# Kernel tuning notes

Hardware: AMD Instinct MI355X
Metric: run time of the kernel (lower is better)

The kernel has to match this reference:

```python
import jax, jax.numpy as jnp
import numpy as np

B, TGT, SRC, SRC_DIM, TGT_DIM = 4, 4096, 4096, 256, 256
NEG_BIG = 1.0e11   # additive mask constant from the torch code
CLAMP_MIN = -1.0e10


def setup_inputs() -> dict:
    key = jax.random.key(0)
    k1, k2, k3, k4 = jax.random.split(key, 4)
    h_t = jax.random.normal(k1, (B, TGT, TGT_DIM), dtype=jnp.float32)
    h_s = jax.random.normal(k2, (B, SRC, SRC_DIM), dtype=jnp.float32)
    m_s = jax.random.randint(k3, (B, SRC), 0, 2, dtype=jnp.int32)
    # linear_in: nn.Linear(src_dim, tgt_dim, bias=False) -> weight [tgt_dim, src_dim]
    lim = float(np.sqrt(1.0 / SRC_DIM))
    W_in = jax.random.uniform(k4, (TGT_DIM, SRC_DIM), dtype=jnp.float32, minval=-lim, maxval=lim)
    return {"h_t": h_t, "h_s": h_s, "m_s": m_s, "W_in": W_in}


def reference(h_t, h_s, m_s, W_in):
    # 'general' score: h_t @ (linear_in(h_s))^T
    energy = jnp.einsum("bsd,td->bst", h_s, W_in)          # (B, S, tgt_dim)
    scores = jnp.einsum("btd,bsd->bts", h_t, energy)        # (B, T, S)
    m = m_s.astype(scores.dtype)[:, None, :]                 # (B, 1, S)
    scores = scores * m - NEG_BIG * (1.0 - m)
    scores = jax.nn.softmax(jnp.maximum(scores, CLAMP_MIN), axis=-1)
    context = jnp.einsum("bts,bsd->btd", scores, h_s)        # (B, T, src_dim)
    return context, scores
```

## Files before the change

kernel.cpp:

```cpp
#include <hip/hip_runtime.h>
#include <cstdint>
#include <cstddef>

typedef _Float16 f16;
typedef _Float16 half8 __attribute__((ext_vector_type(8)));
typedef float floatx4 __attribute__((ext_vector_type(4)));

__device__ __forceinline__ void gload_lds16(const void* g, void* l) {
    __builtin_amdgcn_global_load_lds(
        (const __attribute__((address_space(1))) void*)g,
        (__attribute__((address_space(3))) void*)l,
        16, 0, 0);
}

__global__ void k_cvt(const float* __restrict__ src, f16* __restrict__ dst, int n8) {
    int i = blockIdx.x * blockDim.x + threadIdx.x;
    if (i >= n8) return;
    const float4* s = (const float4*)src + 2 * (size_t)i;
    float4 a = s[0], b = s[1];
    half8 h;
    h[0] = (f16)a.x; h[1] = (f16)a.y; h[2] = (f16)a.z; h[3] = (f16)a.w;
    h[4] = (f16)b.x; h[5] = (f16)b.y; h[6] = (f16)b.z; h[7] = (f16)b.w;
    ((half8*)dst)[i] = h;
}

__global__ void k_hs(const float* __restrict__ hs, f16* __restrict__ hs16, f16* __restrict__ hsT) {
    int id = blockIdx.x;
    int dt = id & 3;
    int st = (id >> 2) & 63;
    int b  = id >> 8;
    __shared__ f16 tile[64][65];
    int t = threadIdx.x;
    int s0 = st * 64, d0 = dt * 64;
#pragma unroll
    for (int i = 0; i < 16; i++) {
        int e = t + i * 256;
        int r = e >> 6, c = e & 63;
        float v = hs[((size_t)(b * 4096 + s0 + r)) * 256 + d0 + c];
        f16 hv = (f16)v;
        hs16[((size_t)(b * 4096 + s0 + r)) * 256 + d0 + c] = hv;
        tile[r][c] = hv;
    }
    __syncthreads();
#pragma unroll
    for (int i = 0; i < 16; i++) {
        int e = t + i * 256;
        int r = e >> 6, c = e & 63;
        hsT[((size_t)(b * 256 + d0 + r)) * 4096 + s0 + c] = tile[c][r];
    }
}

__global__ __launch_bounds__(256, 2) void k_energy(
    const f16* __restrict__ A,
    const f16* __restrict__ Bt,
    f16* __restrict__ C)
{
    int id = blockIdx.x;
    int tn = id & 1, tm = (id >> 1) & 31, b = id >> 6;
    const f16* Ab = A + (size_t)b * 4096 * 256;

    __shared__ __align__(16) f16 As[128 * 64];
    __shared__ __align__(16) f16 Bs[128 * 64];

    int tid = threadIdx.x;
    int wave = tid >> 6, lane = tid & 63;
    int wr = wave >> 1, wc = wave & 1;
    int lm = lane & 15, lq = lane >> 4;

    floatx4 acc[4][4] = {};
    int r0 = tm * 128, c0 = tn * 128;

    for (int k0 = 0; k0 < 256; k0 += 64) {
#pragma unroll
        for (int i = 0; i < 4; i++) {
            int rbase = wave * 32 + i * 8;
            int row = rbase + (lane >> 3);
            gload_lds16(Ab + (size_t)(r0 + row) * 256 + k0 + (lane & 7) * 8, &As[rbase * 64]);
            gload_lds16(Bt + (size_t)(c0 + row) * 256 + k0 + (lane & 7) * 8, &Bs[rbase * 64]);
        }
        __syncthreads();
        half8 af[4][2], bf[4][2];
#pragma unroll
        for (int mi = 0; mi < 4; mi++)
#pragma unroll
            for (int kk = 0; kk < 2; kk++) {
                af[mi][kk] = *(const half8*)&As[(wr * 64 + mi * 16 + lm) * 64 + kk * 32 + lq * 8];
                bf[mi][kk] = *(const half8*)&Bs[(wc * 64 + mi * 16 + lm) * 64 + kk * 32 + lq * 8];
            }
#pragma unroll
        for (int kk = 0; kk < 2; kk++)
#pragma unroll
            for (int mi = 0; mi < 4; mi++)
#pragma unroll
                for (int ni = 0; ni < 4; ni++)
                    acc[mi][ni] = __builtin_amdgcn_mfma_f32_16x16x32_f16(af[mi][kk], bf[ni][kk], acc[mi][ni], 0, 0, 0);
        __syncthreads();
    }
#pragma unroll
    for (int mi = 0; mi < 4; mi++)
#pragma unroll
        for (int ni = 0; ni < 4; ni++)
#pragma unroll
            for (int r = 0; r < 4; r++) {
                int row = r0 + wr * 64 + mi * 16 + lq * 4 + r;
                int col = c0 + wc * 64 + ni * 16 + lm;
                C[(size_t)(b * 4096 + row) * 256 + col] = (f16)acc[mi][ni][r];
            }
}

__global__ __launch_bounds__(256, 2) void k_scores(
    const f16* __restrict__ A,
    const f16* __restrict__ Bt,
    const int* __restrict__ ms,
    float* __restrict__ C,
    float* __restrict__ rsum)
{
    int id = blockIdx.x;
    int tn = id & 31, tm = (id >> 5) & 31, b = id >> 10;
    const f16* Ab = A + (size_t)b * 4096 * 256;
    const f16* Bb = Bt + (size_t)b * 4096 * 256;

    __shared__ __align__(16) f16 As[128 * 64];
    __shared__ __align__(16) f16 Bs[128 * 64];

    int tid = threadIdx.x;
    int wave = tid >> 6, lane = tid & 63;
    int wr = wave >> 1, wc = wave & 1;
    int lm = lane & 15, lq = lane >> 4;

    floatx4 acc[4][4] = {};
    int r0 = tm * 128, c0 = tn * 128;

    for (int k0 = 0; k0 < 256; k0 += 64) {
#pragma unroll
        for (int i = 0; i < 4; i++) {
            int rbase = wave * 32 + i * 8;
            int row = rbase + (lane >> 3);
            gload_lds16(Ab + (size_t)(r0 + row) * 256 + k0 + (lane & 7) * 8, &As[rbase * 64]);
            gload_lds16(Bb + (size_t)(c0 + row) * 256 + k0 + (lane & 7) * 8, &Bs[rbase * 64]);
        }
        __syncthreads();
        half8 af[4][2], bf[4][2];
#pragma unroll
        for (int mi = 0; mi < 4; mi++)
#pragma unroll
            for (int kk = 0; kk < 2; kk++) {
                af[mi][kk] = *(const half8*)&As[(wr * 64 + mi * 16 + lm) * 64 + kk * 32 + lq * 8];
                bf[mi][kk] = *(const half8*)&Bs[(wc * 64 + mi * 16 + lm) * 64 + kk * 32 + lq * 8];
            }
#pragma unroll
        for (int kk = 0; kk < 2; kk++)
#pragma unroll
            for (int mi = 0; mi < 4; mi++)
#pragma unroll
                for (int ni = 0; ni < 4; ni++)
                    acc[mi][ni] = __builtin_amdgcn_mfma_f32_16x16x32_f16(af[mi][kk], bf[ni][kk], acc[mi][ni], 0, 0, 0);
        __syncthreads();
    }
    float rs[4][4] = {};
#pragma unroll
    for (int ni = 0; ni < 4; ni++) {
        int col = c0 + wc * 64 + ni * 16 + lm;
        int m = ms[b * 4096 + col];
#pragma unroll
        for (int mi = 0; mi < 4; mi++)
#pragma unroll
            for (int r = 0; r < 4; r++) {
                int row = r0 + wr * 64 + mi * 16 + lq * 4 + r;
                float v = m ? acc[mi][ni][r] : -1.0e10f;
                C[(size_t)(b * 4096 + row) * 4096 + col] = v;
                rs[mi][r] += __expf(v);
            }
    }
#pragma unroll
    for (int mi = 0; mi < 4; mi++)
#pragma unroll
        for (int r = 0; r < 4; r++) {
            float v = rs[mi][r];
#pragma unroll
            for (int off = 1; off < 16; off <<= 1)
                v += __shfl_xor(v, off, 16);
            if (lm == 0) {
                int row = r0 + wr * 64 + mi * 16 + lq * 4 + r;
                atomicAdd(&rsum[b * 4096 + row], v);
            }
        }
}

__global__ __launch_bounds__(256, 2) void k_ctx(
    const f16* __restrict__ BtT,
    float* __restrict__ Sc,
    const float* __restrict__ rsum,
    float* __restrict__ part)
{
    int id = blockIdx.x;
    int ks = id & 3, tt = (id >> 2) & 31, b = id >> 7;
    int tid = threadIdx.x;
    int wave = tid >> 6, lane = tid & 63;
    int lm = lane & 15, lq = lane >> 4;

    __shared__ __align__(16) f16 Bs[256 * 64];

    int t0 = tt * 128;
    const f16* Bb = BtT + (size_t)b * 256 * 4096;

    float rinv[2];
    size_t rowbase[2];
#pragma unroll
    for (int mi = 0; mi < 2; mi++) {
        int row = t0 + wave * 32 + mi * 16 + lm;
        int gr = b * 4096 + row;
        rinv[mi] = 1.0f / rsum[gr];
        rowbase[mi] = (size_t)gr * 4096;
    }

    floatx4 acc[2][16] = {};
    int sbeg = ks * 1024;

    for (int it = 0; it < 16; it++) {
        int s0 = sbeg + it * 64;
#pragma unroll
        for (int i = 0; i < 8; i++) {
            int rbase = wave * 64 + i * 8;
            gload_lds16(Bb + (size_t)(rbase + (lane >> 3)) * 4096 + s0 + (lane & 7) * 8, &Bs[rbase * 64]);
        }
        half8 af[2][2];
#pragma unroll
        for (int mi = 0; mi < 2; mi++)
#pragma unroll
            for (int kk = 0; kk < 2; kk++) {
                int sidx = s0 + kk * 32 + lq * 8;
                float* p = Sc + rowbase[mi] + sidx;
                float4 v0 = ((const float4*)p)[0];
                float4 v1 = ((const float4*)p)[1];
                float p0 = __expf(v0.x) * rinv[mi];
                float p1 = __expf(v0.y) * rinv[mi];
                float p2 = __expf(v0.z) * rinv[mi];
                float p3 = __expf(v0.w) * rinv[mi];
                float p4 = __expf(v1.x) * rinv[mi];
                float p5 = __expf(v1.y) * rinv[mi];
                float p6 = __expf(v1.z) * rinv[mi];
                float p7 = __expf(v1.w) * rinv[mi];
                ((float4*)p)[0] = make_float4(p0, p1, p2, p3);
                ((float4*)p)[1] = make_float4(p4, p5, p6, p7);
                half8 h;
                h[0] = (f16)p0; h[1] = (f16)p1; h[2] = (f16)p2; h[3] = (f16)p3;
                h[4] = (f16)p4; h[5] = (f16)p5; h[6] = (f16)p6; h[7] = (f16)p7;
                af[mi][kk] = h;
            }
        __syncthreads();
#pragma unroll
        for (int kk = 0; kk < 2; kk++)
#pragma unroll
            for (int ni = 0; ni < 16; ni++) {
                half8 bf = *(const half8*)&Bs[(ni * 16 + lm) * 64 + kk * 32 + lq * 8];
#pragma unroll
                for (int mi = 0; mi < 2; mi++)
                    acc[mi][ni] = __builtin_amdgcn_mfma_f32_16x16x32_f16(af[mi][kk], bf, acc[mi][ni], 0, 0, 0);
            }
        __syncthreads();
    }

    float* P = part + (size_t)ks * 4194304 + (size_t)b * 1048576;
#pragma unroll
    for (int mi = 0; mi < 2; mi++)
#pragma unroll
        for (int ni = 0; ni < 16; ni++)
#pragma unroll
            for (int r = 0; r < 4; r++) {
                int row = t0 + wave * 32 + mi * 16 + lq * 4 + r;
                int col = ni * 16 + lm;
                P[(size_t)row * 256 + col] = acc[mi][ni][r];
            }
}

__global__ void k_red(const float* __restrict__ part, float* __restrict__ out) {
    size_t i = (size_t)blockIdx.x * 256 + threadIdx.x;
    const float4* p = (const float4*)part;
    float4 a = p[i];
    float4 b = p[i + 1048576];
    float4 c = p[i + 2097152];
    float4 d = p[i + 3145728];
    a.x += b.x + c.x + d.x;
    a.y += b.y + c.y + d.y;
    a.z += b.z + c.z + d.z;
    a.w += b.w + c.w + d.w;
    ((float4*)out)[i] = a;
}

extern "C" void kernel_launch(void* const* d_in, const int* in_sizes, int n_in,
                              void* d_out, int out_size, void* d_ws, size_t ws_size,
                              hipStream_t stream) {
    const float* h_t = (const float*)d_in[0];
    const float* h_s = (const float*)d_in[1];
    const int*   m_s = (const int*)d_in[2];
    const float* W   = (const float*)d_in[3];

    float* out = (float*)d_out;
    char* ws = (char*)d_ws;
    f16* h_t16 = (f16*)(ws);
    f16* h_s16 = (f16*)(ws + 8388608);
    f16* h_sT  = (f16*)(ws + 16777216);
    f16* en16  = (f16*)(ws + 25165824);
    f16* W16   = (f16*)(ws + 33554432);
    float* rsum = (float*)(ws + 33685504);
    float* part = (float*)(ws + 33816576);

    float* ctx = out;
    float* sc  = out + 4194304;

    hipMemsetAsync(rsum, 0, 16384 * sizeof(float), stream);
    k_cvt<<<2048, 256, 0, stream>>>(h_t, h_t16, 524288);
    k_cvt<<<32, 256, 0, stream>>>(W, W16, 8192);
    k_hs<<<1024, 256, 0, stream>>>(h_s, h_s16, h_sT);
    k_energy<<<256, 256, 0, stream>>>(h_s16, W16, en16);
    k_scores<<<4096, 256, 0, stream>>>(h_t16, en16, m_s, sc, rsum);
    k_ctx<<<512, 256, 0, stream>>>(h_sT, sc, rsum, part);
    k_red<<<4096, 256, 0, stream>>>(part, ctx);
}
```

Baseline: 570.5 us.

## Store exponentials in score kernel and swizzle LDS layout in context kernel

The score kernel now writes exp(score) (or zero for masked positions) instead of the raw score, so the context kernel only multiplies by the inverse row sum and no longer recomputes exp. The context kernel's LDS tile for the transposed source is reorganised into an XOR-swizzled layout, which is meant to avoid bank conflicts on the MFMA operand reads. Score loads are also issued before the async LDS loads so the two overlap. The stored probabilities are now rounded through fp16 before being written back in fp32, which lowers the precision of the returned scores output.

```diff
diff --git a/kernel.cpp b/kernel.cpp
--- a/kernel.cpp
+++ b/kernel.cpp
@@ -167,9 +167,9 @@
 #pragma unroll
             for (int r = 0; r < 4; r++) {
                 int row = r0 + wr * 64 + mi * 16 + lq * 4 + r;
-                float v = m ? acc[mi][ni][r] : -1.0e10f;
-                C[(size_t)(b * 4096 + row) * 4096 + col] = v;
-                rs[mi][r] += __expf(v);
+                float e = m ? __expf(acc[mi][ni][r]) : 0.0f;
+                C[(size_t)(b * 4096 + row) * 4096 + col] = e;
+                rs[mi][r] += e;
             }
     }
 #pragma unroll
@@ -199,7 +199,7 @@
     int wave = tid >> 6, lane = tid & 63;
     int lm = lane & 15, lq = lane >> 4;
 
-    __shared__ __align__(16) f16 Bs[256 * 64];
+    __shared__ __align__(16) f16 Bs[8 * 2048];
 
     int t0 = tt * 128;
     const f16* Bb = BtT + (size_t)b * 256 * 4096;
@@ -214,46 +214,67 @@
         rowbase[mi] = (size_t)gr * 4096;
     }
 
+    int g0 = wave * 2, g1 = wave * 2 + 1;
+    int c0g = 2 * (g0 & 3), c1g = 2 * (g1 & 3);
+    const f16* gp0 = Bb + (size_t)(lane ^ c0g) * 4096 + g0 * 8;
+    const f16* gp1 = Bb + (size_t)(lane ^ c1g) * 4096 + g1 * 8;
+    f16* lb0 = &Bs[g0 * 2048];
+    f16* lb1 = &Bs[g1 * 2048];
+
+    int rbk[2];
+    rbk[0] = (0 * 4 + lq) * 2048 + (lm ^ (2 * lq)) * 8;
+    rbk[1] = (1 * 4 + lq) * 2048 + (lm ^ (2 * lq)) * 8;
+
     floatx4 acc[2][16] = {};
     int sbeg = ks * 1024;
 
     for (int it = 0; it < 16; it++) {
         int s0 = sbeg + it * 64;
-#pragma unroll
-        for (int i = 0; i < 8; i++) {
-            int rbase = wave * 64 + i * 8;
-            gload_lds16(Bb + (size_t)(rbase + (lane >> 3)) * 4096 + s0 + (lane & 7) * 8, &Bs[rbase * 64]);
+        float4 v[2][2][2];
+#pragma unroll
+        for (int mi = 0; mi < 2; mi++)
+#pragma unroll
+            for (int kk = 0; kk < 2; kk++) {
+                const float* p = Sc + rowbase[mi] + s0 + kk * 32 + lq * 8;
+                v[mi][kk][0] = ((const float4*)p)[0];
+                v[mi][kk][1] = ((const float4*)p)[1];
+            }
+#pragma unroll
+        for (int R = 0; R < 256; R += 64) {
+            gload_lds16(gp0 + (size_t)R * 4096 + s0, lb0 + R * 8);
+            gload_lds16(gp1 + (size_t)R * 4096 + s0, lb1 + R * 8);
         }
         half8 af[2][2];
 #pragma unroll
         for (int mi = 0; mi < 2; mi++)
 #pragma unroll
             for (int kk = 0; kk < 2; kk++) {
-                int sidx = s0 + kk * 32 + lq * 8;
-                float* p = Sc + rowbase[mi] + sidx;
-                float4 v0 = ((const float4*)p)[0];
-                float4 v1 = ((const float4*)p)[1];
-                float p0 = __expf(v0.x) * rinv[mi];
-                float p1 = __expf(v0.y) * rinv[mi];
-                float p2 = __expf(v0.z) * rinv[mi];
-                float p3 = __expf(v0.w) * rinv[mi];
-                float p4 = __expf(v1.x) * rinv[mi];
-                float p5 = __expf(v1.y) * rinv[mi];
-                float p6 = __expf(v1.z) * rinv[mi];
-                float p7 = __expf(v1.w) * rinv[mi];
-                ((float4*)p)[0] = make_float4(p0, p1, p2, p3);
-                ((float4*)p)[1] = make_float4(p4, p5, p6, p7);
                 half8 h;
-                h[0] = (f16)p0; h[1] = (f16)p1; h[2] = (f16)p2; h[3] = (f16)p3;
-                h[4] = (f16)p4; h[5] = (f16)p5; h[6] = (f16)p6; h[7] = (f16)p7;
+                h[0] = (f16)(v[mi][kk][0].x * rinv[mi]);
+                h[1] = (f16)(v[mi][kk][0].y * rinv[mi]);
+                h[2] = (f16)(v[mi][kk][0].z * rinv[mi]);
+                h[3] = (f16)(v[mi][kk][0].w * rinv[mi]);
+                h[4] = (f16)(v[mi][kk][1].x * rinv[mi]);
+                h[5] = (f16)(v[mi][kk][1].y * rinv[mi]);
+                h[6] = (f16)(v[mi][kk][1].z * rinv[mi]);
+                h[7] = (f16)(v[mi][kk][1].w * rinv[mi]);
                 af[mi][kk] = h;
             }
         __syncthreads();
 #pragma unroll
+        for (int mi = 0; mi < 2; mi++)
+#pragma unroll
+            for (int kk = 0; kk < 2; kk++) {
+                float* p = Sc + rowbase[mi] + s0 + kk * 32 + lq * 8;
+                half8 h = af[mi][kk];
+                ((float4*)p)[0] = make_float4((float)h[0], (float)h[1], (float)h[2], (float)h[3]);
+                ((float4*)p)[1] = make_float4((float)h[4], (float)h[5], (float)h[6], (float)h[7]);
+            }
+#pragma unroll
         for (int kk = 0; kk < 2; kk++)
 #pragma unroll
             for (int ni = 0; ni < 16; ni++) {
-                half8 bf = *(const half8*)&Bs[(ni * 16 + lm) * 64 + kk * 32 + lq * 8];
+                half8 bf = *(const half8*)&Bs[rbk[kk] + ni * 128];
 #pragma unroll
                 for (int mi = 0; mi < 2; mi++)
                     acc[mi][ni] = __builtin_amdgcn_mfma_f32_16x16x32_f16(af[mi][kk], bf, acc[mi][ni], 0, 0, 0);
```

Result: faster. 542.7 us (-4.9%).
